# Kernel tuning notes

Measured on AMD Instinct MI355X. Metric: run time of the kernel, lower is better.

The kernel has to match this reference:

```python
import jax, jax.numpy as jnp
import numpy as np

B, S, H, F, E, K = 2, 1024, 2048, 5504, 8, 2


def setup_inputs() -> dict:
    key = jax.random.key(0)
    k0, k1, k2, k3, k4 = jax.random.split(key, 5)
    x = jax.random.normal(k0, (B, S, H), dtype=jnp.float32)
    # nn.Linear weight layout is [out, in]
    router_w = jax.random.normal(k1, (E, H), dtype=jnp.float32) * 0.02   # router gate
    gate_w = jax.random.normal(k2, (E, F, H), dtype=jnp.float32) * 0.02  # per-expert gate_proj
    up_w = jax.random.normal(k3, (E, F, H), dtype=jnp.float32) * 0.02    # per-expert up_proj
    down_w = jax.random.normal(k4, (E, H, F), dtype=jnp.float32) * 0.02  # per-expert down_proj
    return {"x": x, "router_w": router_w, "gate_w": gate_w, "up_w": up_w, "down_w": down_w}


def reference(x, router_w, gate_w, up_w, down_w):
    b, s, h = x.shape
    xf = x.reshape(-1, h)                                   # [T, H]
    # --- router: top-k over expert logits, softmax over the k selected ---
    logits = xf @ router_w.T                                # [T, E]
    top_v, top_i = jax.lax.top_k(logits, K)                 # [T, K]
    probs = jax.nn.softmax(top_v.astype(jnp.float32), axis=-1).astype(logits.dtype)
    # per-token combine weight for each expert (0 if not selected)
    combine = jnp.sum(jax.nn.one_hot(top_i, E, dtype=x.dtype) * probs[..., None], axis=1)  # [T, E]
    # --- experts: SwiGLU, batched over the expert axis ---
    g = jnp.einsum('th,efh->etf', xf, gate_w)               # [E, T, F]
    u = jnp.einsum('th,efh->etf', xf, up_w)                 # [E, T, F]
    y = jnp.einsum('etf,ehf->eth', jax.nn.silu(g) * u, down_w)  # [E, T, H]
    # --- combine: weighted sum over experts ---
    out = jnp.einsum('te,eth->th', combine, y)              # [T, H]
    return out.reshape(b, s, h)
```

## Files before the change

### kernel.cpp

```cpp
#include <hip/hip_runtime.h>
#include <cstdint>
#include <cstddef>

#define H 2048
#define F 5504
#define E 8
#define T 2048
#define ROWCAP 5120

#define BM 128
#define BN 128
#define BK 32

typedef __bf16 bf16x8 __attribute__((ext_vector_type(8)));
typedef float f32x4 __attribute__((ext_vector_type(4)));

#define AS1(p) ((const __attribute__((address_space(1))) void*)(p))
#define AS3(p) ((__attribute__((address_space(3))) void*)(p))

__global__ void router_kernel(const float* __restrict__ x,
                              const float* __restrict__ rw,
                              int* __restrict__ cnt,
                              int* __restrict__ list_t,
                              float* __restrict__ list_w) {
    const int wv = threadIdx.x >> 6;
    const int lane = threadIdx.x & 63;
    const int t = blockIdx.x * 4 + wv;
    const float4* xp = (const float4*)(x + (size_t)t * H) + lane * 8;
    float4 xv[8];
#pragma unroll
    for (int i = 0; i < 8; ++i) xv[i] = xp[i];
    float lg[E];
#pragma unroll
    for (int e = 0; e < E; ++e) {
        const float4* wp = (const float4*)(rw + (size_t)e * H) + lane * 8;
        float acc = 0.f;
#pragma unroll
        for (int i = 0; i < 8; ++i) {
            float4 w4 = wp[i];
            acc += xv[i].x * w4.x + xv[i].y * w4.y + xv[i].z * w4.z + xv[i].w * w4.w;
        }
#pragma unroll
        for (int o = 32; o > 0; o >>= 1) acc += __shfl_xor(acc, o, 64);
        lg[e] = acc;
    }
    if (lane == 0) {
        float v0 = -3e38f, v1 = -3e38f;
        int i0 = 0, i1 = 0;
#pragma unroll
        for (int e = 0; e < E; ++e) {
            float v = lg[e];
            if (v > v0) { v1 = v0; i1 = i0; v0 = v; i0 = e; }
            else if (v > v1) { v1 = v; i1 = e; }
        }
        float p0 = 1.f / (1.f + __expf(v1 - v0));
        float p1 = 1.f - p0;
        int s0 = atomicAdd(&cnt[i0], 1);
        list_t[i0 * T + s0] = t;
        list_w[i0 * T + s0] = p0;
        int s1 = atomicAdd(&cnt[i1], 1);
        list_t[i1 * T + s1] = t;
        list_w[i1 * T + s1] = p1;
    }
}

__global__ void offsets_kernel(const int* __restrict__ cnt, int* __restrict__ off) {
    if (threadIdx.x == 0) {
        int acc = 0;
        for (int e = 0; e < E; ++e) {
            off[e] = acc;
            acc += (cnt[e] + 127) & ~127;
        }
    }
}

__global__ void gather_kernel(const float* __restrict__ x,
                              const int* __restrict__ cnt,
                              const int* __restrict__ off,
                              const int* __restrict__ list_t,
                              const float* __restrict__ list_w,
                              __bf16* __restrict__ Abuf,
                              int* __restrict__ row_t,
                              float* __restrict__ row_w) {
    const int e = blockIdx.y, slot = blockIdx.x;
    if (slot >= cnt[e]) return;
    const int row = off[e] + slot;
    if (threadIdx.x == 0) {
        row_t[row] = list_t[e * T + slot];
        row_w[row] = list_w[e * T + slot];
    }
    const int t = list_t[e * T + slot];
    const float4* src = (const float4*)(x + (size_t)t * H);
    float4 a = src[threadIdx.x * 2], b = src[threadIdx.x * 2 + 1];
    bf16x8 o;
    o[0] = (__bf16)a.x; o[1] = (__bf16)a.y; o[2] = (__bf16)a.z; o[3] = (__bf16)a.w;
    o[4] = (__bf16)b.x; o[5] = (__bf16)b.y; o[6] = (__bf16)b.z; o[7] = (__bf16)b.w;
    *(bf16x8*)(Abuf + (size_t)row * H + threadIdx.x * 8) = o;
}

__global__ void __launch_bounds__(256, 2)
gateup_kernel(const __bf16* __restrict__ Abuf,
              const float* __restrict__ gw,
              const float* __restrict__ uw,
              const int* __restrict__ cnt,
              const int* __restrict__ off,
              const float* __restrict__ row_w,
              __bf16* __restrict__ act) {
    const int e = blockIdx.z;
    const int count = cnt[e];
    const int mt = blockIdx.y;
    if (mt * BM >= count) return;
    const int n0 = blockIdx.x * BN;
    const int rowbase = off[e] + mt * BM;

    __shared__ __bf16 As0[BM * BK], As1[BM * BK];
    __shared__ __bf16 Gs0[BN * BK], Gs1[BN * BK];
    __shared__ __bf16 Us0[BN * BK], Us1[BN * BK];

    const int tid = threadIdx.x;
    const int wv = tid >> 6, lane = tid & 63;
    const int wr = wv >> 1, wc = wv & 1;
    const int quad = lane >> 4, l16 = lane & 15;

    f32x4 accG[4][4] = {};
    f32x4 accU[4][4] = {};

    const __bf16* abase = Abuf + (size_t)rowbase * H;
    const float* gbase = gw + (size_t)e * F * H + (size_t)n0 * H;
    const float* ubase = uw + (size_t)e * F * H + (size_t)n0 * H;

    const int arow = lane >> 2;
    const int acol = (lane & 3) * 8;
    const int wrow = tid >> 1;
    const int kh = (tid & 1) * 16;

    float4 pg[4], pu[4];

#define STAGE_A(AS, k0)                                                                  \
    do {                                                                                 \
        _Pragma("unroll")                                                                \
        for (int i_ = 0; i_ < 2; ++i_) {                                                 \
            const int seg_ = wv * 2 + i_;                                                \
            const __bf16* gp_ = abase + (size_t)(seg_ * 16 + arow) * H + (k0) + acol;    \
            __builtin_amdgcn_global_load_lds(AS1(gp_), AS3(AS + seg_ * 512), 16, 0, 0);  \
        }                                                                                \
    } while (0)

#define LOAD_W(k0)                                                                   \
    do {                                                                             \
        const float4* gp_ = (const float4*)(gbase + (size_t)wrow * H + (k0) + kh);   \
        pg[0] = gp_[0]; pg[1] = gp_[1]; pg[2] = gp_[2]; pg[3] = gp_[3];              \
        const float4* up_ = (const float4*)(ubase + (size_t)wrow * H + (k0) + kh);   \
        pu[0] = up_[0]; pu[1] = up_[1]; pu[2] = up_[2]; pu[3] = up_[3];              \
    } while (0)

#define WRITE_W(GS, US)                                                                          \
    do {                                                                                         \
        bf16x8 h0_, h1_;                                                                         \
        h0_[0] = (__bf16)pg[0].x; h0_[1] = (__bf16)pg[0].y; h0_[2] = (__bf16)pg[0].z; h0_[3] = (__bf16)pg[0].w; \
        h0_[4] = (__bf16)pg[1].x; h0_[5] = (__bf16)pg[1].y; h0_[6] = (__bf16)pg[1].z; h0_[7] = (__bf16)pg[1].w; \
        h1_[0] = (__bf16)pg[2].x; h1_[1] = (__bf16)pg[2].y; h1_[2] = (__bf16)pg[2].z; h1_[3] = (__bf16)pg[2].w; \
        h1_[4] = (__bf16)pg[3].x; h1_[5] = (__bf16)pg[3].y; h1_[6] = (__bf16)pg[3].z; h1_[7] = (__bf16)pg[3].w; \
        *(bf16x8*)(GS + wrow * BK + kh) = h0_;                                                   \
        *(bf16x8*)(GS + wrow * BK + kh + 8) = h1_;                                               \
        h0_[0] = (__bf16)pu[0].x; h0_[1] = (__bf16)pu[0].y; h0_[2] = (__bf16)pu[0].z; h0_[3] = (__bf16)pu[0].w; \
        h0_[4] = (__bf16)pu[1].x; h0_[5] = (__bf16)pu[1].y; h0_[6] = (__bf16)pu[1].z; h0_[7] = (__bf16)pu[1].w; \
        h1_[0] = (__bf16)pu[2].x; h1_[1] = (__bf16)pu[2].y; h1_[2] = (__bf16)pu[2].z; h1_[3] = (__bf16)pu[2].w; \
        h1_[4] = (__bf16)pu[3].x; h1_[5] = (__bf16)pu[3].y; h1_[6] = (__bf16)pu[3].z; h1_[7] = (__bf16)pu[3].w; \
        *(bf16x8*)(US + wrow * BK + kh) = h0_;                                                   \
        *(bf16x8*)(US + wrow * BK + kh + 8) = h1_;                                               \
    } while (0)

#define COMPUTE(AS, GS, US)                                                                      \
    do {                                                                                         \
        bf16x8 af_[4], gf_[4], uf_[4];                                                           \
        _Pragma("unroll")                                                                        \
        for (int i_ = 0; i_ < 4; ++i_)                                                           \
            af_[i_] = *(const bf16x8*)(AS + (wr * 64 + i_ * 16 + l16) * BK + quad * 8);          \
        _Pragma("unroll")                                                                        \
        for (int j_ = 0; j_ < 4; ++j_) {                                                         \
            gf_[j_] = *(const bf16x8*)(GS + (wc * 64 + j_ * 16 + l16) * BK + quad * 8);          \
            uf_[j_] = *(const bf16x8*)(US + (wc * 64 + j_ * 16 + l16) * BK + quad * 8);          \
        }                                                                                        \
        _Pragma("unroll")                                                                        \
        for (int i_ = 0; i_ < 4; ++i_)                                                           \
            _Pragma("unroll")                                                                    \
            for (int j_ = 0; j_ < 4; ++j_) {                                                     \
                accG[i_][j_] = __builtin_amdgcn_mfma_f32_16x16x32_bf16(af_[i_], gf_[j_], accG[i_][j_], 0, 0, 0); \
                accU[i_][j_] = __builtin_amdgcn_mfma_f32_16x16x32_bf16(af_[i_], uf_[j_], accU[i_][j_], 0, 0, 0); \
            }                                                                                    \
    } while (0)

    STAGE_A(As0, 0);
    LOAD_W(0);
    WRITE_W(Gs0, Us0);
    __syncthreads();

    const int NT = H / BK;
    for (int t = 0; t < NT; t += 2) {
        STAGE_A(As1, (t + 1) * BK);
        LOAD_W((t + 1) * BK);
        COMPUTE(As0, Gs0, Us0);
        WRITE_W(Gs1, Us1);
        __syncthreads();
        if (t + 2 < NT) {
            STAGE_A(As0, (t + 2) * BK);
            LOAD_W((t + 2) * BK);
        }
        COMPUTE(As1, Gs1, Us1);
        if (t + 2 < NT) WRITE_W(Gs0, Us0);
        __syncthreads();
    }

#undef STAGE_A
#undef LOAD_W
#undef WRITE_W
#undef COMPUTE

#pragma unroll
    for (int i = 0; i < 4; ++i) {
        const int ml = wr * 64 + i * 16 + quad * 4;
#pragma unroll
        for (int r = 0; r < 4; ++r) {
            const float w = row_w[rowbase + ml + r];
            __bf16* arow_p = act + (size_t)(rowbase + ml + r) * F + n0;
#pragma unroll
            for (int j = 0; j < 4; ++j) {
                const int nl = wc * 64 + j * 16 + l16;
                float g = accG[i][j][r], u = accU[i][j][r];
                float s = g / (1.f + __expf(-g));
                arow_p[nl] = (__bf16)(s * u * w);
            }
        }
    }
}

__global__ void __launch_bounds__(256, 2)
down_kernel(const __bf16* __restrict__ act,
            const float* __restrict__ dw,
            const int* __restrict__ cnt,
            const int* __restrict__ off,
            const int* __restrict__ row_t,
              float* __restrict__ out) {
    const int e = blockIdx.z;
    const int count = cnt[e];
    const int mt = blockIdx.y;
    if (mt * BM >= count) return;
    const int h0 = blockIdx.x * BN;
    const int rowbase = off[e] + mt * BM;

    __shared__ __bf16 As0[BM * BK], As1[BM * BK];
    __shared__ __bf16 Ws0[BN * BK], Ws1[BN * BK];

    const int tid = threadIdx.x;
    const int wv = tid >> 6, lane = tid & 63;
    const int wr = wv >> 1, wc = wv & 1;
    const int quad = lane >> 4, l16 = lane & 15;

    f32x4 acc[4][4] = {};

    const __bf16* abase = act + (size_t)rowbase * F;
    const float* wbase = dw + (size_t)e * H * F + (size_t)h0 * F;

    const int arow = lane >> 2;
    const int acol = (lane & 3) * 8;
    const int wrow = tid >> 1;
    const int kh = (tid & 1) * 16;

    float4 pw[4];

#define STAGE_A(AS, k0)                                                                  \
    do {                                                                                 \
        _Pragma("unroll")                                                                \
        for (int i_ = 0; i_ < 2; ++i_) {                                                 \
            const int seg_ = wv * 2 + i_;                                                \
            const __bf16* gp_ = abase + (size_t)(seg_ * 16 + arow) * F + (k0) + acol;    \
            __builtin_amdgcn_global_load_lds(AS1(gp_), AS3(AS + seg_ * 512), 16, 0, 0);  \
        }                                                                                \
    } while (0)

#define LOAD_W(k0)                                                                   \
    do {                                                                             \
        const float4* gp_ = (const float4*)(wbase + (size_t)wrow * F + (k0) + kh);   \
        pw[0] = gp_[0]; pw[1] = gp_[1]; pw[2] = gp_[2]; pw[3] = gp_[3];              \
    } while (0)

#define WRITE_W(WS)                                                                              \
    do {                                                                                         \
        bf16x8 h0_, h1_;                                                                         \
        h0_[0] = (__bf16)pw[0].x; h0_[1] = (__bf16)pw[0].y; h0_[2] = (__bf16)pw[0].z; h0_[3] = (__bf16)pw[0].w; \
        h0_[4] = (__bf16)pw[1].x; h0_[5] = (__bf16)pw[1].y; h0_[6] = (__bf16)pw[1].z; h0_[7] = (__bf16)pw[1].w; \
        h1_[0] = (__bf16)pw[2].x; h1_[1] = (__bf16)pw[2].y; h1_[2] = (__bf16)pw[2].z; h1_[3] = (__bf16)pw[2].w; \
        h1_[4] = (__bf16)pw[3].x; h1_[5] = (__bf16)pw[3].y; h1_[6] = (__bf16)pw[3].z; h1_[7] = (__bf16)pw[3].w; \
        *(bf16x8*)(WS + wrow * BK + kh) = h0_;                                                   \
        *(bf16x8*)(WS + wrow * BK + kh + 8) = h1_;                                               \
    } while (0)

#define COMPUTE(AS, WS)                                                                          \
    do {                                                                                         \
        bf16x8 af_[4], bf_[4];                                                                   \
        _Pragma("unroll")                                                                        \
        for (int i_ = 0; i_ < 4; ++i_)                                                           \
            af_[i_] = *(const bf16x8*)(AS + (wr * 64 + i_ * 16 + l16) * BK + quad * 8);          \
        _Pragma("unroll")                                                                        \
        for (int j_ = 0; j_ < 4; ++j_)                                                           \
            bf_[j_] = *(const bf16x8*)(WS + (wc * 64 + j_ * 16 + l16) * BK + quad * 8);          \
        _Pragma("unroll")                                                                        \
        for (int i_ = 0; i_ < 4; ++i_)                                                           \
            _Pragma("unroll")                                                                    \
            for (int j_ = 0; j_ < 4; ++j_)                                                       \
                acc[i_][j_] = __builtin_amdgcn_mfma_f32_16x16x32_bf16(af_[i_], bf_[j_], acc[i_][j_], 0, 0, 0); \
    } while (0)

    STAGE_A(As0, 0);
    LOAD_W(0);
    WRITE_W(Ws0);
    __syncthreads();

    const int NT = F / BK;
    for (int t = 0; t < NT; t += 2) {
        STAGE_A(As1, (t + 1) * BK);
        LOAD_W((t + 1) * BK);
        COMPUTE(As0, Ws0);
        WRITE_W(Ws1);
        __syncthreads();
        if (t + 2 < NT) {
            STAGE_A(As0, (t + 2) * BK);
            LOAD_W((t + 2) * BK);
        }
        COMPUTE(As1, Ws1);
        if (t + 2 < NT) WRITE_W(Ws0);
        __syncthreads();
    }

#undef STAGE_A
#undef LOAD_W
#undef WRITE_W
#undef COMPUTE

#pragma unroll
    for (int i = 0; i < 4; ++i) {
        const int ml = wr * 64 + i * 16 + quad * 4;
#pragma unroll
        for (int r = 0; r < 4; ++r) {
            const int lr = mt * BM + ml + r;
            if (lr < count) {
                const int t = row_t[rowbase + ml + r];
                float* orow = out + (size_t)t * H + h0;
#pragma unroll
                for (int j = 0; j < 4; ++j)
                    atomicAdd(&orow[wc * 64 + j * 16 + l16], acc[i][j][r]);
            }
        }
    }
}

extern "C" void kernel_launch(void* const* d_in, const int* in_sizes, int n_in,
                              void* d_out, int out_size, void* d_ws, size_t ws_size,
                              hipStream_t stream) {
    const float* x  = (const float*)d_in[0];
    const float* rw = (const float*)d_in[1];
    const float* gw = (const float*)d_in[2];
    const float* uw = (const float*)d_in[3];
    const float* dw = (const float*)d_in[4];
    float* out = (float*)d_out;
    char* ws = (char*)d_ws;

    int*   cnt    = (int*)(ws + 0);
    int*   off    = (int*)(ws + 256);
    int*   list_t = (int*)(ws + 1024);
    float* list_w = (float*)(ws + 1024 + 65536);
    int*   row_t  = (int*)(ws + 1024 + 2 * 65536);
    float* row_w  = (float*)(ws + 1024 + 2 * 65536 + ROWCAP * 4);
    __bf16* Abuf  = (__bf16*)(ws + 262144);
    __bf16* act   = (__bf16*)(ws + 262144 + (size_t)ROWCAP * H * 2);

    hipMemsetAsync(d_out, 0, (size_t)out_size * sizeof(float), stream);
    hipMemsetAsync(ws, 0, 1024, stream);

    router_kernel<<<T / 4, 256, 0, stream>>>(x, rw, cnt, list_t, list_w);
    offsets_kernel<<<1, 64, 0, stream>>>(cnt, off);
    gather_kernel<<<dim3(T, E), 256, 0, stream>>>(x, cnt, off, list_t, list_w, Abuf, row_t, row_w);
    gateup_kernel<<<dim3(F / BN, T / BM, E), 256, 0, stream>>>(Abuf, gw, uw, cnt, off, row_w, act);
    down_kernel<<<dim3(H / BN, T / BM, E), 256, 0, stream>>>(act, dw, cnt, off, row_t, out);
}
```

Baseline: 1.664 ms.

## Pre-convert expert weights to bf16 and use async global-to-LDS loads in GEMMs

Adds a conversion kernel that casts all gate, up and down expert weights to bf16 in workspace on every call. New GEMM kernels then stream bf16 tiles straight into LDS with global_load_lds and run MFMA on them. The aim is to halve weight bytes read inside the GEMMs and drop the per-tile fp32-to-bf16 conversion. In exchange, each call pays an extra full pass that reads the fp32 weights and writes bf16 copies, and the new path only runs if the workspace is large enough.

```diff
diff --git a/kernel.cpp b/kernel.cpp
--- a/kernel.cpp
+++ b/kernel.cpp
@@ -98,14 +98,228 @@
     *(bf16x8*)(Abuf + (size_t)row * H + threadIdx.x * 8) = o;
 }
 
+__global__ void convw_kernel(const float* __restrict__ s0, const float* __restrict__ s1,
+                             const float* __restrict__ s2,
+                             __bf16* __restrict__ d0, __bf16* __restrict__ d1,
+                             __bf16* __restrict__ d2) {
+    const float* s = blockIdx.y == 0 ? s0 : (blockIdx.y == 1 ? s1 : s2);
+    __bf16* d = blockIdx.y == 0 ? d0 : (blockIdx.y == 1 ? d1 : d2);
+    const size_t n = (size_t)E * F * H;
+    size_t i = ((size_t)blockIdx.x * blockDim.x + threadIdx.x) * 8;
+    const size_t stride = (size_t)gridDim.x * blockDim.x * 8;
+    for (; i < n; i += stride) {
+        float4 a = *(const float4*)(s + i);
+        float4 b = *(const float4*)(s + i + 4);
+        bf16x8 o;
+        o[0] = (__bf16)a.x; o[1] = (__bf16)a.y; o[2] = (__bf16)a.z; o[3] = (__bf16)a.w;
+        o[4] = (__bf16)b.x; o[5] = (__bf16)b.y; o[6] = (__bf16)b.z; o[7] = (__bf16)b.w;
+        *(bf16x8*)(d + i) = o;
+    }
+}
+
+__global__ void __launch_bounds__(256, 3)
+gateup_bf16k(const __bf16* __restrict__ Abuf,
+             const __bf16* __restrict__ gwb,
+             const __bf16* __restrict__ uwb,
+             const int* __restrict__ cnt,
+             const int* __restrict__ off,
+             const float* __restrict__ row_w,
+             __bf16* __restrict__ act) {
+    const int e = blockIdx.z;
+    const int count = cnt[e];
+    const int mt = blockIdx.y;
+    if (mt * BM >= count) return;
+    const int n0 = blockIdx.x * BN;
+    const int rowbase = off[e] + mt * BM;
+
+    __shared__ __bf16 As0[BM * BK], As1[BM * BK];
+    __shared__ __bf16 Gs0[BN * BK], Gs1[BN * BK];
+    __shared__ __bf16 Us0[BN * BK], Us1[BN * BK];
+
+    const int tid = threadIdx.x;
+    const int wv = tid >> 6, lane = tid & 63;
+    const int wr = wv >> 1, wc = wv & 1;
+    const int quad = lane >> 4, l16 = lane & 15;
+
+    f32x4 accG[4][4] = {};
+    f32x4 accU[4][4] = {};
+
+    const __bf16* abase = Abuf + (size_t)rowbase * H;
+    const __bf16* gbase = gwb + (size_t)e * F * H + (size_t)n0 * H;
+    const __bf16* ubase = uwb + (size_t)e * F * H + (size_t)n0 * H;
+
+    const int arow = lane >> 2;
+    const int acol = (lane & 3) * 8;
+
+#define STAGE(AS, GS, US, k0)                                                                \
+    do {                                                                                     \
+        _Pragma("unroll")                                                                    \
+        for (int i_ = 0; i_ < 2; ++i_) {                                                     \
+            const int seg_ = wv * 2 + i_;                                                    \
+            const size_t roff_ = (size_t)(seg_ * 16 + arow);                                 \
+            __builtin_amdgcn_global_load_lds(AS1(abase + roff_ * H + (k0) + acol),           \
+                                             AS3(AS + seg_ * 512), 16, 0, 0);               \
+            __builtin_amdgcn_global_load_lds(AS1(gbase + roff_ * H + (k0) + acol),           \
+                                             AS3(GS + seg_ * 512), 16, 0, 0);               \
+            __builtin_amdgcn_global_load_lds(AS1(ubase + roff_ * H + (k0) + acol),           \
+                                             AS3(US + seg_ * 512), 16, 0, 0);               \
+        }                                                                                    \
+    } while (0)
+
+#define COMPUTE(AS, GS, US)                                                                      \
+    do {                                                                                         \
+        bf16x8 af_[4], gf_[4], uf_[4];                                                           \
+        _Pragma("unroll")                                                                        \
+        for (int i_ = 0; i_ < 4; ++i_)                                                           \
+            af_[i_] = *(const bf16x8*)(AS + (wr * 64 + i_ * 16 + l16) * BK + quad * 8);          \
+        _Pragma("unroll")                                                                        \
+        for (int j_ = 0; j_ < 4; ++j_) {                                                         \
+            gf_[j_] = *(const bf16x8*)(GS + (wc * 64 + j_ * 16 + l16) * BK + quad * 8);          \
+            uf_[j_] = *(const bf16x8*)(US + (wc * 64 + j_ * 16 + l16) * BK + quad * 8);          \
+        }                                                                                        \
+        _Pragma("unroll")                                                                        \
+        for (int i_ = 0; i_ < 4; ++i_)                                                           \
+            _Pragma("unroll")                                                                    \
+            for (int j_ = 0; j_ < 4; ++j_) {                                                     \
+                accG[i_][j_] = __builtin_amdgcn_mfma_f32_16x16x32_bf16(af_[i_], gf_[j_], accG[i_][j_], 0, 0, 0); \
+                accU[i_][j_] = __builtin_amdgcn_mfma_f32_16x16x32_bf16(af_[i_], uf_[j_], accU[i_][j_], 0, 0, 0); \
+            }                                                                                    \
+    } while (0)
+
+    STAGE(As0, Gs0, Us0, 0);
+    __syncthreads();
+
+    const int NT = H / BK;
+    for (int t = 0; t < NT; t += 2) {
+        STAGE(As1, Gs1, Us1, (t + 1) * BK);
+        COMPUTE(As0, Gs0, Us0);
+        __syncthreads();
+        if (t + 2 < NT) STAGE(As0, Gs0, Us0, (t + 2) * BK);
+        COMPUTE(As1, Gs1, Us1);
+        __syncthreads();
+    }
+
+#undef STAGE
+#undef COMPUTE
+
+#pragma unroll
+    for (int i = 0; i < 4; ++i) {
+        const int ml = wr * 64 + i * 16 + quad * 4;
+#pragma unroll
+        for (int r = 0; r < 4; ++r) {
+            const float w = row_w[rowbase + ml + r];
+            __bf16* arow_p = act + (size_t)(rowbase + ml + r) * F + n0;
+#pragma unroll
+            for (int j = 0; j < 4; ++j) {
+                const int nl = wc * 64 + j * 16 + l16;
+                float g = accG[i][j][r], u = accU[i][j][r];
+                float s = g / (1.f + __expf(-g));
+                arow_p[nl] = (__bf16)(s * u * w);
+            }
+        }
+    }
+}
+
+__global__ void __launch_bounds__(256, 4)
+down_bf16k(const __bf16* __restrict__ act,
+           const __bf16* __restrict__ dwb,
+           const int* __restrict__ cnt,
+           const int* __restrict__ off,
+           const int* __restrict__ row_t,
+           float* __restrict__ out) {
+    const int e = blockIdx.z;
+    const int count = cnt[e];
+    const int mt = blockIdx.y;
+    if (mt * BM >= count) return;
+    const int h0 = blockIdx.x * BN;
+    const int rowbase = off[e] + mt * BM;
+
+    __shared__ __bf16 As0[BM * BK], As1[BM * BK];
+    __shared__ __bf16 Ws0[BN * BK], Ws1[BN * BK];
+
+    const int tid = threadIdx.x;
+    const int wv = tid >> 6, lane = tid & 63;
+    const int wr = wv >> 1, wc = wv & 1;
+    const int quad = lane >> 4, l16 = lane & 15;
+
+    f32x4 acc[4][4] = {};
+
+    const __bf16* abase = act + (size_t)rowbase * F;
+    const __bf16* wbase = dwb + (size_t)e * H * F + (size_t)h0 * F;
+
+    const int arow = lane >> 2;
+    const int acol = (lane & 3) * 8;
+
+#define STAGE(AS, WS, k0)                                                                    \
+    do {                                                                                     \
+        _Pragma("unroll")                                                                    \
+        for (int i_ = 0; i_ < 2; ++i_) {                                                     \
+            const int seg_ = wv * 2 + i_;                                                    \
+            const size_t roff_ = (size_t)(seg_ * 16 + arow);                                 \
+            __builtin_amdgcn_global_load_lds(AS1(abase + roff_ * F + (k0) + acol),           \
+                                             AS3(AS + seg_ * 512), 16, 0, 0);               \
+            __builtin_amdgcn_global_load_lds(AS1(wbase + roff_ * F + (k0) + acol),           \
+                                             AS3(WS + seg_ * 512), 16, 0, 0);               \
+        }                                                                                    \
+    } while (0)
+
+#define COMPUTE(AS, WS)                                                                          \
+    do {                                                                                         \
+        bf16x8 af_[4], bf_[4];                                                                   \
+        _Pragma("unroll")                                                                        \
+        for (int i_ = 0; i_ < 4; ++i_)                                                           \
+            af_[i_] = *(const bf16x8*)(AS + (wr * 64 + i_ * 16 + l16) * BK + quad * 8);          \
+        _Pragma("unroll")                                                                        \
+        for (int j_ = 0; j_ < 4; ++j_)                                                           \
+            bf_[j_] = *(const bf16x8*)(WS + (wc * 64 + j_ * 16 + l16) * BK + quad * 8);          \
+        _Pragma("unroll")                                                                        \
+        for (int i_ = 0; i_ < 4; ++i_)                                                           \
+            _Pragma("unroll")                                                                    \
+            for (int j_ = 0; j_ < 4; ++j_)                                                       \
+                acc[i_][j_] = __builtin_amdgcn_mfma_f32_16x16x32_bf16(af_[i_], bf_[j_], acc[i_][j_], 0, 0, 0); \
+    } while (0)
+
+    STAGE(As0, Ws0, 0);
+    __syncthreads();
+
+    const int NT = F / BK;
+    for (int t = 0; t < NT; t += 2) {
+        STAGE(As1, Ws1, (t + 1) * BK);
+        COMPUTE(As0, Ws0);
+        __syncthreads();
+        if (t + 2 < NT) STAGE(As0, Ws0, (t + 2) * BK);
+        COMPUTE(As1, Ws1);
+        __syncthreads();
+    }
+
+#undef STAGE
+#undef COMPUTE
+
+#pragma unroll
+    for (int i = 0; i < 4; ++i) {
+        const int ml = wr * 64 + i * 16 + quad * 4;
+#pragma unroll
+        for (int r = 0; r < 4; ++r) {
+            const int lr = mt * BM + ml + r;
+            if (lr < count) {
+                const int t = row_t[rowbase + ml + r];
+                float* orow = out + (size_t)t * H + h0;
+#pragma unroll
+                for (int j = 0; j < 4; ++j)
+                    atomicAdd(&orow[wc * 64 + j * 16 + l16], acc[i][j][r]);
+            }
+        }
+    }
+}
+
 __global__ void __launch_bounds__(256, 2)
-gateup_kernel(const __bf16* __restrict__ Abuf,
-              const float* __restrict__ gw,
-              const float* __restrict__ uw,
-              const int* __restrict__ cnt,
-              const int* __restrict__ off,
-              const float* __restrict__ row_w,
-              __bf16* __restrict__ act) {
+gateup_f32k(const __bf16* __restrict__ Abuf,
+            const float* __restrict__ gw,
+            const float* __restrict__ uw,
+            const int* __restrict__ cnt,
+            const int* __restrict__ off,
+            const float* __restrict__ row_w,
+            __bf16* __restrict__ act) {
     const int e = blockIdx.z;
     const int count = cnt[e];
     const int mt = blockIdx.y;
@@ -236,12 +450,12 @@
 }
 
 __global__ void __launch_bounds__(256, 2)
-down_kernel(const __bf16* __restrict__ act,
-            const float* __restrict__ dw,
-            const int* __restrict__ cnt,
-            const int* __restrict__ off,
-            const int* __restrict__ row_t,
-              float* __restrict__ out) {
+down_f32k(const __bf16* __restrict__ act,
+          const float* __restrict__ dw,
+          const int* __restrict__ cnt,
+          const int* __restrict__ off,
+          const int* __restrict__ row_t,
+          float* __restrict__ out) {
     const int e = blockIdx.z;
     const int count = cnt[e];
     const int mt = blockIdx.y;
@@ -372,8 +586,15 @@
     float* list_w = (float*)(ws + 1024 + 65536);
     int*   row_t  = (int*)(ws + 1024 + 2 * 65536);
     float* row_w  = (float*)(ws + 1024 + 2 * 65536 + ROWCAP * 4);
-    __bf16* Abuf  = (__bf16*)(ws + 262144);
-    __bf16* act   = (__bf16*)(ws + 262144 + (size_t)ROWCAP * H * 2);
+
+    const size_t ABUF_OFF = 262144;
+    const size_t ACT_OFF  = ABUF_OFF + (size_t)ROWCAP * H * 2;
+    const size_t WGB_OFF  = ACT_OFF + (size_t)ROWCAP * F * 2;
+    const size_t WSZ      = (size_t)E * F * H * 2;
+    const size_t NEED     = WGB_OFF + 3 * WSZ;
+
+    __bf16* Abuf = (__bf16*)(ws + ABUF_OFF);
+    __bf16* act  = (__bf16*)(ws + ACT_OFF);
 
     hipMemsetAsync(d_out, 0, (size_t)out_size * sizeof(float), stream);
     hipMemsetAsync(ws, 0, 1024, stream);
@@ -381,6 +602,16 @@
     router_kernel<<<T / 4, 256, 0, stream>>>(x, rw, cnt, list_t, list_w);
     offsets_kernel<<<1, 64, 0, stream>>>(cnt, off);
     gather_kernel<<<dim3(T, E), 256, 0, stream>>>(x, cnt, off, list_t, list_w, Abuf, row_t, row_w);
-    gateup_kernel<<<dim3(F / BN, T / BM, E), 256, 0, stream>>>(Abuf, gw, uw, cnt, off, row_w, act);
-    down_kernel<<<dim3(H / BN, T / BM, E), 256, 0, stream>>>(act, dw, cnt, off, row_t, out);
-}
+
+    if (ws_size >= NEED) {
+        __bf16* wgb = (__bf16*)(ws + WGB_OFF);
+        __bf16* wub = (__bf16*)(ws + WGB_OFF + WSZ);
+        __bf16* wdb = (__bf16*)(ws + WGB_OFF + 2 * WSZ);
+        convw_kernel<<<dim3(2048, 3), 256, 0, stream>>>(gw, uw, dw, wgb, wub, wdb);
+        gateup_bf16k<<<dim3(F / BN, T / BM, E), 256, 0, stream>>>(Abuf, wgb, wub, cnt, off, row_w, act);
+        down_bf16k<<<dim3(H / BN, T / BM, E), 256, 0, stream>>>(act, wdb, cnt, off, row_t, out);
+    } else {
+        gateup_f32k<<<dim3(F / BN, T / BM, E), 256, 0, stream>>>(Abuf, gw, uw, cnt, off, row_w, act);
+        down_f32k<<<dim3(H / BN, T / BM, E), 256, 0, stream>>>(act, dw, cnt, off, row_t, out);
+    }
+}
```

Measured after the change: 2.611 ms. 56.9% more time.

## Split-K down projection, widen K tile to 64 with XOR-swizzled LDS

Applied to the files above, without the earlier changes.

The down-projection kernel now splits the F reduction into two halves across blocks, doubling the grid, and relies on the existing atomicAdd epilogue to merge partial sums. The K tile grows from 32 to 64, with XOR swizzling on the A and W shared-memory layouts to avoid bank conflicts. The aim is more parallelism, fewer barriers per unit of work and cheaper LDS reads. In exchange it doubles the atomic traffic to the output and doubles LDS use per block, which may reduce occupancy.

```diff
diff --git a/kernel.cpp b/kernel.cpp
--- a/kernel.cpp
+++ b/kernel.cpp
@@ -11,6 +11,8 @@
 #define BM 128
 #define BN 128
 #define BK 32
+#define DBK 64
+
 
 typedef __bf16 bf16x8 __attribute__((ext_vector_type(8)));
 typedef float f32x4 __attribute__((ext_vector_type(4)));
@@ -241,16 +243,18 @@
             const int* __restrict__ cnt,
             const int* __restrict__ off,
             const int* __restrict__ row_t,
-              float* __restrict__ out) {
+            float* __restrict__ out) {
     const int e = blockIdx.z;
     const int count = cnt[e];
     const int mt = blockIdx.y;
     if (mt * BM >= count) return;
-    const int h0 = blockIdx.x * BN;
+    const int h0 = (blockIdx.x & 15) * BN;
+    const int ksl = blockIdx.x >> 4;
+    const int kbase = ksl * (F / 2);
     const int rowbase = off[e] + mt * BM;
 
-    __shared__ __bf16 As0[BM * BK], As1[BM * BK];
-    __shared__ __bf16 Ws0[BN * BK], Ws1[BN * BK];
+    __shared__ __bf16 As0[BM * DBK], As1[BM * DBK];
+    __shared__ __bf16 Ws0[BN * DBK], Ws1[BN * DBK];
 
     const int tid = threadIdx.x;
     const int wv = tid >> 6, lane = tid & 63;
@@ -262,81 +266,92 @@
     const __bf16* abase = act + (size_t)rowbase * F;
     const float* wbase = dw + (size_t)e * H * F + (size_t)h0 * F;
 
-    const int arow = lane >> 2;
-    const int acol = (lane & 3) * 8;
+    const int arow8 = lane >> 3;
+    const int ascol = ((lane & 7) ^ arow8) * 8;
     const int wrow = tid >> 1;
-    const int kh = (tid & 1) * 16;
-
-    float4 pw[4];
-
-#define STAGE_A(AS, k0)                                                                  \
+    const int kh = (tid & 1) * 32;
+
+    float4 pw[8];
+
+#define DSTAGE_A(AS, k0)                                                                 \
     do {                                                                                 \
         _Pragma("unroll")                                                                \
-        for (int i_ = 0; i_ < 2; ++i_) {                                                 \
-            const int seg_ = wv * 2 + i_;                                                \
-            const __bf16* gp_ = abase + (size_t)(seg_ * 16 + arow) * F + (k0) + acol;    \
+        for (int i_ = 0; i_ < 4; ++i_) {                                                 \
+            const int seg_ = wv * 4 + i_;                                                \
+            const __bf16* gp_ = abase + (size_t)(seg_ * 8 + arow8) * F + (k0) + ascol;   \
             __builtin_amdgcn_global_load_lds(AS1(gp_), AS3(AS + seg_ * 512), 16, 0, 0);  \
         }                                                                                \
     } while (0)
 
-#define LOAD_W(k0)                                                                   \
+#define DLOAD_W(k0)                                                                  \
     do {                                                                             \
         const float4* gp_ = (const float4*)(wbase + (size_t)wrow * F + (k0) + kh);   \
-        pw[0] = gp_[0]; pw[1] = gp_[1]; pw[2] = gp_[2]; pw[3] = gp_[3];              \
-    } while (0)
-
-#define WRITE_W(WS)                                                                              \
+        _Pragma("unroll")                                                            \
+        for (int j_ = 0; j_ < 8; ++j_) pw[j_] = gp_[j_];                             \
+    } while (0)
+
+#define DWRITE_W(WS)                                                                             \
     do {                                                                                         \
-        bf16x8 h0_, h1_;                                                                         \
-        h0_[0] = (__bf16)pw[0].x; h0_[1] = (__bf16)pw[0].y; h0_[2] = (__bf16)pw[0].z; h0_[3] = (__bf16)pw[0].w; \
-        h0_[4] = (__bf16)pw[1].x; h0_[5] = (__bf16)pw[1].y; h0_[6] = (__bf16)pw[1].z; h0_[7] = (__bf16)pw[1].w; \
-        h1_[0] = (__bf16)pw[2].x; h1_[1] = (__bf16)pw[2].y; h1_[2] = (__bf16)pw[2].z; h1_[3] = (__bf16)pw[2].w; \
-        h1_[4] = (__bf16)pw[3].x; h1_[5] = (__bf16)pw[3].y; h1_[6] = (__bf16)pw[3].z; h1_[7] = (__bf16)pw[3].w; \
-        *(bf16x8*)(WS + wrow * BK + kh) = h0_;                                                   \
-        *(bf16x8*)(WS + wrow * BK + kh + 8) = h1_;                                               \
-    } while (0)
-
-#define COMPUTE(AS, WS)                                                                          \
+        _Pragma("unroll")                                                                        \
+        for (int j8_ = 0; j8_ < 4; ++j8_) {                                                      \
+            float4 a_ = pw[2 * j8_], b_ = pw[2 * j8_ + 1];                                       \
+            bf16x8 h_;                                                                           \
+            h_[0] = (__bf16)a_.x; h_[1] = (__bf16)a_.y; h_[2] = (__bf16)a_.z; h_[3] = (__bf16)a_.w; \
+            h_[4] = (__bf16)b_.x; h_[5] = (__bf16)b_.y; h_[6] = (__bf16)b_.z; h_[7] = (__bf16)b_.w; \
+            const int slot_ = ((tid & 1) * 4 + j8_) ^ (wrow & 7);                                \
+            *(bf16x8*)(WS + wrow * DBK + slot_ * 8) = h_;                                        \
+        }                                                                                        \
+    } while (0)
+
+#define DCOMPUTE(AS, WS)                                                                         \
     do {                                                                                         \
-        bf16x8 af_[4], bf_[4];                                                                   \
         _Pragma("unroll")                                                                        \
-        for (int i_ = 0; i_ < 4; ++i_)                                                           \
-            af_[i_] = *(const bf16x8*)(AS + (wr * 64 + i_ * 16 + l16) * BK + quad * 8);          \
-        _Pragma("unroll")                                                                        \
-        for (int j_ = 0; j_ < 4; ++j_)                                                           \
-            bf_[j_] = *(const bf16x8*)(WS + (wc * 64 + j_ * 16 + l16) * BK + quad * 8);          \
-        _Pragma("unroll")                                                                        \
-        for (int i_ = 0; i_ < 4; ++i_)                                                           \
+        for (int ks2_ = 0; ks2_ < 2; ++ks2_) {                                                   \
+            bf16x8 af_[4], bf_[4];                                                               \
             _Pragma("unroll")                                                                    \
-            for (int j_ = 0; j_ < 4; ++j_)                                                       \
-                acc[i_][j_] = __builtin_amdgcn_mfma_f32_16x16x32_bf16(af_[i_], bf_[j_], acc[i_][j_], 0, 0, 0); \
-    } while (0)
-
-    STAGE_A(As0, 0);
-    LOAD_W(0);
-    WRITE_W(Ws0);
+            for (int i_ = 0; i_ < 4; ++i_) {                                                     \
+                const int r_ = wr * 64 + i_ * 16 + l16;                                          \
+                af_[i_] = *(const bf16x8*)(AS + r_ * DBK + ((ks2_ * 4 + quad) ^ (r_ & 7)) * 8);  \
+            }                                                                                    \
+            _Pragma("unroll")                                                                    \
+            for (int j_ = 0; j_ < 4; ++j_) {                                                     \
+                const int r_ = wc * 64 + j_ * 16 + l16;                                          \
+                bf_[j_] = *(const bf16x8*)(WS + r_ * DBK + ((ks2_ * 4 + quad) ^ (r_ & 7)) * 8);  \
+            }                                                                                    \
+            _Pragma("unroll")                                                                    \
+            for (int i_ = 0; i_ < 4; ++i_)                                                       \
+                _Pragma("unroll")                                                                \
+                for (int j_ = 0; j_ < 4; ++j_)                                                   \
+                    acc[i_][j_] = __builtin_amdgcn_mfma_f32_16x16x32_bf16(af_[i_], bf_[j_], acc[i_][j_], 0, 0, 0); \
+        }                                                                                        \
+    } while (0)
+
+    DSTAGE_A(As0, kbase);
+    DLOAD_W(kbase);
+    DWRITE_W(Ws0);
     __syncthreads();
 
-    const int NT = F / BK;
-    for (int t = 0; t < NT; t += 2) {
-        STAGE_A(As1, (t + 1) * BK);
-        LOAD_W((t + 1) * BK);
-        COMPUTE(As0, Ws0);
-        WRITE_W(Ws1);
+    const int NT = (F / 2) / DBK;
+    for (int t = 0; t < NT - 1; t += 2) {
+        DSTAGE_A(As1, kbase + (t + 1) * DBK);
+        DLOAD_W(kbase + (t + 1) * DBK);
+        DCOMPUTE(As0, Ws0);
+        DWRITE_W(Ws1);
         __syncthreads();
         if (t + 2 < NT) {
-            STAGE_A(As0, (t + 2) * BK);
-            LOAD_W((t + 2) * BK);
-        }
-        COMPUTE(As1, Ws1);
-        if (t + 2 < NT) WRITE_W(Ws0);
+            DSTAGE_A(As0, kbase + (t + 2) * DBK);
+            DLOAD_W(kbase + (t + 2) * DBK);
+        }
+        DCOMPUTE(As1, Ws1);
+        if (t + 2 < NT) DWRITE_W(Ws0);
         __syncthreads();
     }
-
-#undef STAGE_A
-#undef LOAD_W
-#undef WRITE_W
-#undef COMPUTE
+    DCOMPUTE(As0, Ws0);
+
+#undef DSTAGE_A
+#undef DLOAD_W
+#undef DWRITE_W
+#undef DCOMPUTE
 
 #pragma unroll
     for (int i = 0; i < 4; ++i) {
@@ -382,5 +397,5 @@
     offsets_kernel<<<1, 64, 0, stream>>>(cnt, off);
     gather_kernel<<<dim3(T, E), 256, 0, stream>>>(x, cnt, off, list_t, list_w, Abuf, row_t, row_w);
     gateup_kernel<<<dim3(F / BN, T / BM, E), 256, 0, stream>>>(Abuf, gw, uw, cnt, off, row_w, act);
-    down_kernel<<<dim3(H / BN, T / BM, E), 256, 0, stream>>>(act, dw, cnt, off, row_t, out);
-}
+    down_kernel<<<dim3(32, T / BM, E), 256, 0, stream>>>(act, dw, cnt, off, row_t, out);
+}
```

Measured after the change: 1.599 ms. -3.9%, faster.
